# Optimization experiments

Hardware: AMD Instinct MI355X
Metric: run time of the kernel (lower is better)

## Reference

```python
import jax, jax.numpy as jnp
import numpy as np

# RoIAlign config (matches init_kwargs)
OUT_H = OUT_W = 7
SPATIAL_SCALE = 0.25
SAMPLING_RATIO = 2  # fixed grid per bin (aligned=True, detectron2-style)
N_IMG, C, H, W = 2, 256, 200, 304
N_ROIS = 512


def setup_inputs() -> dict:
    key = jax.random.key(0)
    kf, kb, kx1, ky1, kw, kh = jax.random.split(key, 6)
    features = jax.random.normal(kf, (N_IMG, C, H, W), dtype=jnp.float32)
    # rois: [R,5] = (batch_idx, x1, y1, x2, y2) in input-image coords (image ~ 1216x800)
    bidx = jax.random.randint(kb, (N_ROIS,), 0, N_IMG).astype(jnp.float32)
    x1 = jax.random.uniform(kx1, (N_ROIS,), minval=0.0, maxval=1100.0)
    y1 = jax.random.uniform(ky1, (N_ROIS,), minval=0.0, maxval=700.0)
    bw = jax.random.uniform(kw, (N_ROIS,), minval=8.0, maxval=116.0)
    bh = jax.random.uniform(kh, (N_ROIS,), minval=8.0, maxval=100.0)
    rois = jnp.stack([bidx, x1, y1, x1 + bw, y1 + bh], axis=1).astype(jnp.float32)
    return {"features": features, "rois": rois}


def roi_align(features, rois):
    N, C_, H_, W_ = features.shape
    G = SAMPLING_RATIO
    b = rois[:, 0].astype(jnp.int32)
    # aligned=True: scale then shift by -0.5 (continuous pixel model)
    x1 = rois[:, 1] * SPATIAL_SCALE - 0.5
    y1 = rois[:, 2] * SPATIAL_SCALE - 0.5
    x2 = rois[:, 3] * SPATIAL_SCALE - 0.5
    y2 = rois[:, 4] * SPATIAL_SCALE - 0.5
    roi_w = x2 - x1  # aligned: no clamp to min 1
    roi_h = y2 - y1
    bin_w = roi_w / OUT_W
    bin_h = roi_h / OUT_H

    # sample coordinates: per roi, OUT*G points along each axis
    iy = jnp.arange(OUT_H * G)
    ix = jnp.arange(OUT_W * G)
    # y = y1 + ph*bin_h + (s+0.5)*bin_h/G
    ys = y1[:, None] + (iy // G) * bin_h[:, None] + ((iy % G) + 0.5) * bin_h[:, None] / G  # [R, OUT_H*G]
    xs = x1[:, None] + (ix // G) * bin_w[:, None] + ((ix % G) + 0.5) * bin_w[:, None] / G  # [R, OUT_W*G]

    y = ys[:, :, None]  # [R, Py, 1]
    x = xs[:, None, :]  # [R, 1, Px]
    valid = ((y > -1.0) & (y < H_) & (x > -1.0) & (x < W_)).astype(features.dtype)  # [R,Py,Px]

    yc = jnp.clip(y, 0.0, H_ - 1)
    xc = jnp.clip(x, 0.0, W_ - 1)
    y0 = jnp.floor(yc).astype(jnp.int32)
    x0 = jnp.floor(xc).astype(jnp.int32)
    y1i = jnp.minimum(y0 + 1, H_ - 1)
    x1i = jnp.minimum(x0 + 1, W_ - 1)
    ly = yc - y0
    lx = xc - x0
    hy = 1.0 - ly
    hx = 1.0 - lx

    badv = b[:, None, None]
    Py, Px = OUT_H * G, OUT_W * G
    y0b = jnp.broadcast_to(y0, (rois.shape[0], Py, Px))
    y1b = jnp.broadcast_to(y1i, (rois.shape[0], Py, Px))
    x0b = jnp.broadcast_to(x0, (rois.shape[0], Py, Px))
    x1b = jnp.broadcast_to(x1i, (rois.shape[0], Py, Px))

    # advanced indexing: [R,Py,Px,C]
    v00 = features[badv, :, y0b, x0b]
    v01 = features[badv, :, y0b, x1b]
    v10 = features[badv, :, y1b, x0b]
    v11 = features[badv, :, y1b, x1b]

    w00 = (hy * hx) * valid
    w01 = (hy * lx) * valid
    w10 = (ly * hx) * valid
    w11 = (ly * lx) * valid

    samp = (w00[..., None] * v00 + w01[..., None] * v01 +
            w10[..., None] * v10 + w11[..., None] * v11)  # [R,Py,Px,C]
    # average pool over the GxG samples per bin
    R = rois.shape[0]
    out = samp.reshape(R, OUT_H, G, OUT_W, G, C_).mean(axis=(2, 4))  # [R,OUT_H,OUT_W,C]
    return jnp.transpose(out, (0, 3, 1, 2))  # [R,C,OUT_H,OUT_W]


def reference(features, rois):
    return roi_align(features, rois)
```

## Files before the change

### kernel.cpp

```cpp
#include <hip/hip_runtime.h>


#define OUT_H 7
#define OUT_W 7
constexpr float SPATIAL_SCALE = 0.25f;
constexpr int CN = 256;
constexpr int FH = 200;
constexpr int FW = 304;
constexpr int N_IMG = 2;
constexpr int N_ROIS = 512;
constexpr int PIX = FH * FW;
constexpr size_t PLANE = (size_t)PIX;
constexpr size_t NHWC_ELEMS = (size_t)N_IMG * PLANE * CN;
constexpr size_t NHWC_BF16_BYTES = NHWC_ELEMS * sizeof(unsigned short);

constexpr int CT = 64;
constexpr int PT = 128;

__device__ __forceinline__ unsigned short f2bf_rne(float f) {
    unsigned int u = __float_as_uint(f);
    unsigned int r = (u + 0x7FFFu + ((u >> 16) & 1u)) >> 16;
    return (unsigned short)r;
}

__global__ __launch_bounds__(256) void nchw_to_nhwc_bf16_tiled(
    const float* __restrict__ in, unsigned short* __restrict__ ws)
{
    const int pbase = blockIdx.x * PT;
    const int nc = blockIdx.y;
    const int n = nc >> 2;
    const int cbase = (nc & 3) * CT;

    __shared__ float tile[CT][PT + 1];

    {
        const int q = threadIdx.x & 31;
        const int r = threadIdx.x >> 5;
        const float* src = in + ((size_t)n * CN + cbase) * PLANE + pbase + 4 * q;
#pragma unroll
        for (int i = 0; i < 8; ++i) {
            const int c = r + 8 * i;
            const float4 v = *(const float4*)(src + (size_t)c * PLANE);
            tile[c][4 * q + 0] = v.x;
            tile[c][4 * q + 1] = v.y;
            tile[c][4 * q + 2] = v.z;
            tile[c][4 * q + 3] = v.w;
        }
    }
    __syncthreads();
    {
        const int cq = threadIdx.x & 7;
        const int p0 = threadIdx.x >> 3;
        unsigned short* dstbase =
            ws + ((size_t)n * PLANE + pbase) * CN + cbase + 8 * cq;
#pragma unroll
        for (int i2 = 0; i2 < 4; ++i2) {
            const int p = p0 + 32 * i2;
            uint4 pk;
            pk.x = (unsigned int)f2bf_rne(tile[8 * cq + 0][p]) |
                   ((unsigned int)f2bf_rne(tile[8 * cq + 1][p]) << 16);
            pk.y = (unsigned int)f2bf_rne(tile[8 * cq + 2][p]) |
                   ((unsigned int)f2bf_rne(tile[8 * cq + 3][p]) << 16);
            pk.z = (unsigned int)f2bf_rne(tile[8 * cq + 4][p]) |
                   ((unsigned int)f2bf_rne(tile[8 * cq + 5][p]) << 16);
            pk.w = (unsigned int)f2bf_rne(tile[8 * cq + 6][p]) |
                   ((unsigned int)f2bf_rne(tile[8 * cq + 7][p]) << 16);
            *(uint4*)(dstbase + (size_t)p * CN) = pk;
        }
    }
}

__global__ __launch_bounds__(128) void roi_align_nhwc_bf16(
    const unsigned short* __restrict__ ws,
    const float* __restrict__ rois,
    float* __restrict__ out)
{
    const int b = blockIdx.x;
    const int x = b & 7;
    const int sid = b >> 3;
    const int half = sid & 1;
    const int ph = (sid >> 1) % 7;
    const int r  = ((sid >> 1) / 7) * 8 + x;
    const int t  = threadIdx.x;

    __shared__ float s_roi[5];
    __shared__ int   s_off[16][4];
    __shared__ float s_w[16][4];
    __shared__ int   s_b;

    if (t < 5) s_roi[t] = rois[r * 5 + t];
    __syncthreads();

    const int NW = half ? 6 : 8;
    const int NS = 2 * NW;
    if (t < NS) {
        const int gy  = (t >= NW) ? 1 : 0;
        const int ixl = t - gy * NW;
        const int ix  = half * 8 + ixl;
        const float x1 = s_roi[1] * SPATIAL_SCALE - 0.5f;
        const float y1 = s_roi[2] * SPATIAL_SCALE - 0.5f;
        const float x2 = s_roi[3] * SPATIAL_SCALE - 0.5f;
        const float y2 = s_roi[4] * SPATIAL_SCALE - 0.5f;
        const float bin_w = (x2 - x1) / OUT_W;
        const float bin_h = (y2 - y1) / OUT_H;
        const float y = y1 + ph * bin_h + (gy + 0.5f) * bin_h * 0.5f;
        const float xf = x1 + (ix >> 1) * bin_w + ((ix & 1) + 0.5f) * bin_w * 0.5f;
        const float validf =
            (y > -1.0f && y < (float)FH && xf > -1.0f && xf < (float)FW) ? 1.0f : 0.0f;
        const float yc = fminf(fmaxf(y, 0.0f), (float)(FH - 1));
        const float xc = fminf(fmaxf(xf, 0.0f), (float)(FW - 1));
        const int y0 = (int)floorf(yc);
        const int x0 = (int)floorf(xc);
        const int y1i = min(y0 + 1, FH - 1);
        const int x1i = min(x0 + 1, FW - 1);
        const float ly = yc - (float)y0;
        const float lx = xc - (float)x0;
        const float hy = 1.0f - ly;
        const float hx = 1.0f - lx;
        s_off[t][0] = ((y0  * FW + x0 ) * CN) * 2;
        s_off[t][1] = ((y0  * FW + x1i) * CN) * 2;
        s_off[t][2] = ((y1i * FW + x0 ) * CN) * 2;
        s_off[t][3] = ((y1i * FW + x1i) * CN) * 2;
        s_w[t][0] = hy * hx * validf;
        s_w[t][1] = hy * lx * validf;
        s_w[t][2] = ly * hx * validf;
        s_w[t][3] = ly * lx * validf;
    }
    if (t == 0) s_b = (int)s_roi[0];
    __syncthreads();

    const char* base =
        (const char*)(ws + (size_t)s_b * (PLANE * CN) + 2 * t);

    float acc0[4] = {0.f, 0.f, 0.f, 0.f};
    float acc1[4] = {0.f, 0.f, 0.f, 0.f};

    if (half == 0) {
#pragma unroll
        for (int s = 0; s < 16; ++s) {
            const int pw = (s & 7) >> 1;
#pragma unroll
            for (int k = 0; k < 4; ++k) {
                const unsigned int u = *(const unsigned int*)(base + s_off[s][k]);
                const float f0 = __uint_as_float(u << 16);
                const float f1 = __uint_as_float(u & 0xFFFF0000u);
                const float w = s_w[s][k];
                acc0[pw] = fmaf(w, f0, acc0[pw]);
                acc1[pw] = fmaf(w, f1, acc1[pw]);
            }
        }
    } else {
#pragma unroll
        for (int s = 0; s < 12; ++s) {
            const int pw = (s % 6) >> 1;
#pragma unroll
            for (int k = 0; k < 4; ++k) {
                const unsigned int u = *(const unsigned int*)(base + s_off[s][k]);
                const float f0 = __uint_as_float(u << 16);
                const float f1 = __uint_as_float(u & 0xFFFF0000u);
                const float w = s_w[s][k];
                acc0[pw] = fmaf(w, f0, acc0[pw]);
                acc1[pw] = fmaf(w, f1, acc1[pw]);
            }
        }
    }

    const int pw0 = half ? 4 : 0;
    const int npw = half ? 3 : 4;
    const size_t outbase = ((size_t)r * CN + 2 * t) * (OUT_H * OUT_W)
                         + (size_t)ph * OUT_W + pw0;
    for (int pw = 0; pw < npw; ++pw) {
        out[outbase + pw] = acc0[pw] * 0.25f;
        out[outbase + (OUT_H * OUT_W) + pw] = acc1[pw] * 0.25f;
    }
}

__global__ __launch_bounds__(256) void roi_align_nchw(
    const float* __restrict__ feat,
    const float* __restrict__ rois,
    float* __restrict__ out)
{
    const int r  = blockIdx.x;
    const int ph = blockIdx.y;
    const int c  = threadIdx.x;

    __shared__ float s_roi[5];
    __shared__ int   s_off[28][4];
    __shared__ float s_w[28][4];
    __shared__ int   s_b;

    if (threadIdx.x < 5) s_roi[threadIdx.x] = rois[r * 5 + threadIdx.x];
    __syncthreads();

    if (threadIdx.x < 28) {
        const int s  = threadIdx.x;
        const int gy = s / 14;
        const int ix = s % 14;
        const float x1 = s_roi[1] * SPATIAL_SCALE - 0.5f;
        const float y1 = s_roi[2] * SPATIAL_SCALE - 0.5f;
        const float x2 = s_roi[3] * SPATIAL_SCALE - 0.5f;
        const float y2 = s_roi[4] * SPATIAL_SCALE - 0.5f;
        const float bin_w = (x2 - x1) / OUT_W;
        const float bin_h = (y2 - y1) / OUT_H;
        const float y = y1 + ph * bin_h + (gy + 0.5f) * bin_h * 0.5f;
        const float xf = x1 + (ix >> 1) * bin_w + ((ix & 1) + 0.5f) * bin_w * 0.5f;
        const float validf =
            (y > -1.0f && y < (float)FH && xf > -1.0f && xf < (float)FW) ? 1.0f : 0.0f;
        const float yc = fminf(fmaxf(y, 0.0f), (float)(FH - 1));
        const float xc = fminf(fmaxf(xf, 0.0f), (float)(FW - 1));
        const int y0 = (int)floorf(yc);
        const int x0 = (int)floorf(xc);
        const int y1i = min(y0 + 1, FH - 1);
        const int x1i = min(x0 + 1, FW - 1);
        const float ly = yc - (float)y0;
        const float lx = xc - (float)x0;
        const float hy = 1.0f - ly;
        const float hx = 1.0f - lx;
        s_off[s][0] = y0  * FW + x0;
        s_off[s][1] = y0  * FW + x1i;
        s_off[s][2] = y1i * FW + x0;
        s_off[s][3] = y1i * FW + x1i;
        s_w[s][0] = hy * hx * validf;
        s_w[s][1] = hy * lx * validf;
        s_w[s][2] = ly * hx * validf;
        s_w[s][3] = ly * lx * validf;
    }
    if (threadIdx.x == 0) s_b = (int)s_roi[0];
    __syncthreads();

    const float* base = feat + ((size_t)s_b * CN + c) * PLANE;

    float acc[OUT_W] = {0.f, 0.f, 0.f, 0.f, 0.f, 0.f, 0.f};
#pragma unroll
    for (int s = 0; s < 28; ++s) {
        const float v0 = base[s_off[s][0]];
        const float v1 = base[s_off[s][1]];
        const float v2 = base[s_off[s][2]];
        const float v3 = base[s_off[s][3]];
        acc[(s % 14) >> 1] += s_w[s][0] * v0 + s_w[s][1] * v1 +
                              s_w[s][2] * v2 + s_w[s][3] * v3;
    }

    const size_t outbase = ((size_t)r * CN + c) * (OUT_H * OUT_W) + (size_t)ph * OUT_W;
#pragma unroll
    for (int pw = 0; pw < OUT_W; ++pw) {
        out[outbase + pw] = acc[pw] * 0.25f;
    }
}

extern "C" void kernel_launch(void* const* d_in, const int* in_sizes, int n_in,
                              void* d_out, int out_size, void* d_ws, size_t ws_size,
                              hipStream_t stream) {
    const float* feat = (const float*)d_in[0];
    const float* rois = (const float*)d_in[1];
    float* out = (float*)d_out;

    if (ws_size >= NHWC_BF16_BYTES) {
        unsigned short* ws = (unsigned short*)d_ws;
        dim3 tgrid(PIX / PT, (N_IMG * CN) / CT, 1);
        nchw_to_nhwc_bf16_tiled<<<tgrid, dim3(256, 1, 1), 0, stream>>>(feat, ws);
        roi_align_nhwc_bf16<<<dim3(N_ROIS * OUT_H * 2, 1, 1), dim3(128, 1, 1), 0, stream>>>(
            ws, rois, out);
    } else {
        dim3 grid(N_ROIS, OUT_H, 1);
        roi_align_nchw<<<grid, dim3(256, 1, 1), 0, stream>>>(feat, rois, out);
    }
}
```

Measured before the change: 234.6 us.

## Process two output rows and four channels per thread in RoIAlign kernel

```diff
diff --git a/kernel.cpp b/kernel.cpp
--- a/kernel.cpp
+++ b/kernel.cpp
@@ -70,7 +70,7 @@
     }
 }
 
-__global__ __launch_bounds__(128) void roi_align_nhwc_bf16(
+__global__ __launch_bounds__(64) void roi_align_nhwc_bf16(
     const unsigned short* __restrict__ ws,
     const float* __restrict__ rois,
     float* __restrict__ out)
@@ -78,25 +78,26 @@
     const int b = blockIdx.x;
     const int x = b & 7;
     const int sid = b >> 3;
-    const int half = sid & 1;
-    const int ph = (sid >> 1) % 7;
-    const int r  = ((sid >> 1) / 7) * 8 + x;
+    const int r    = (sid >> 2) * 8 + x;
+    const int pair = sid & 3;
+    const int ph0  = 2 * pair;
     const int t  = threadIdx.x;
 
     __shared__ float s_roi[5];
-    __shared__ int   s_off[16][4];
-    __shared__ float s_w[16][4];
+    __shared__ int   s_off[56][4];
+    __shared__ float s_w[56][4];
     __shared__ int   s_b;
 
     if (t < 5) s_roi[t] = rois[r * 5 + t];
     __syncthreads();
 
-    const int NW = half ? 6 : 8;
-    const int NS = 2 * NW;
+    const int NS = (pair < 3) ? 56 : 28;
     if (t < NS) {
-        const int gy  = (t >= NW) ? 1 : 0;
-        const int ixl = t - gy * NW;
-        const int ix  = half * 8 + ixl;
+        const int row = t / 28;
+        const int ss  = t % 28;
+        const int gy = ss / 14;
+        const int ix = ss % 14;
+        const int ph = ph0 + row;
         const float x1 = s_roi[1] * SPATIAL_SCALE - 0.5f;
         const float y1 = s_roi[2] * SPATIAL_SCALE - 0.5f;
         const float x2 = s_roi[3] * SPATIAL_SCALE - 0.5f;
@@ -130,48 +131,69 @@
     __syncthreads();
 
     const char* base =
-        (const char*)(ws + (size_t)s_b * (PLANE * CN) + 2 * t);
-
-    float acc0[4] = {0.f, 0.f, 0.f, 0.f};
-    float acc1[4] = {0.f, 0.f, 0.f, 0.f};
-
-    if (half == 0) {
-#pragma unroll
-        for (int s = 0; s < 16; ++s) {
-            const int pw = (s & 7) >> 1;
+        (const char*)(ws + (size_t)s_b * (PLANE * CN)) + 8 * t;
+
+    float acc0[14] = {0.f,0.f,0.f,0.f,0.f,0.f,0.f,0.f,0.f,0.f,0.f,0.f,0.f,0.f};
+    float acc1[14] = {0.f,0.f,0.f,0.f,0.f,0.f,0.f,0.f,0.f,0.f,0.f,0.f,0.f,0.f};
+    float acc2[14] = {0.f,0.f,0.f,0.f,0.f,0.f,0.f,0.f,0.f,0.f,0.f,0.f,0.f,0.f};
+    float acc3[14] = {0.f,0.f,0.f,0.f,0.f,0.f,0.f,0.f,0.f,0.f,0.f,0.f,0.f,0.f};
+
+    if (pair < 3) {
+#pragma unroll
+        for (int s = 0; s < 56; ++s) {
+            const int ai = (s / 28) * 7 + (((s % 28) % 14) >> 1);
 #pragma unroll
             for (int k = 0; k < 4; ++k) {
-                const unsigned int u = *(const unsigned int*)(base + s_off[s][k]);
-                const float f0 = __uint_as_float(u << 16);
-                const float f1 = __uint_as_float(u & 0xFFFF0000u);
+                const uint2 u = *(const uint2*)(base + s_off[s][k]);
+                const float f0 = __uint_as_float(u.x << 16);
+                const float f1 = __uint_as_float(u.x & 0xFFFF0000u);
+                const float f2 = __uint_as_float(u.y << 16);
+                const float f3 = __uint_as_float(u.y & 0xFFFF0000u);
                 const float w = s_w[s][k];
-                acc0[pw] = fmaf(w, f0, acc0[pw]);
-                acc1[pw] = fmaf(w, f1, acc1[pw]);
+                acc0[ai] = fmaf(w, f0, acc0[ai]);
+                acc1[ai] = fmaf(w, f1, acc1[ai]);
+                acc2[ai] = fmaf(w, f2, acc2[ai]);
+                acc3[ai] = fmaf(w, f3, acc3[ai]);
             }
         }
     } else {
 #pragma unroll
-        for (int s = 0; s < 12; ++s) {
-            const int pw = (s % 6) >> 1;
+        for (int s = 0; s < 28; ++s) {
+            const int ai = (s % 14) >> 1;
 #pragma unroll
             for (int k = 0; k < 4; ++k) {
-                const unsigned int u = *(const unsigned int*)(base + s_off[s][k]);
-                const float f0 = __uint_as_float(u << 16);
-                const float f1 = __uint_as_float(u & 0xFFFF0000u);
+                const uint2 u = *(const uint2*)(base + s_off[s][k]);
+                const float f0 = __uint_as_float(u.x << 16);
+                const float f1 = __uint_as_float(u.x & 0xFFFF0000u);
+                const float f2 = __uint_as_float(u.y << 16);
+                const float f3 = __uint_as_float(u.y & 0xFFFF0000u);
                 const float w = s_w[s][k];
-                acc0[pw] = fmaf(w, f0, acc0[pw]);
-                acc1[pw] = fmaf(w, f1, acc1[pw]);
+                acc0[ai] = fmaf(w, f0, acc0[ai]);
+                acc1[ai] = fmaf(w, f1, acc1[ai]);
+                acc2[ai] = fmaf(w, f2, acc2[ai]);
+                acc3[ai] = fmaf(w, f3, acc3[ai]);
             }
         }
     }
 
-    const int pw0 = half ? 4 : 0;
-    const int npw = half ? 3 : 4;
-    const size_t outbase = ((size_t)r * CN + 2 * t) * (OUT_H * OUT_W)
-                         + (size_t)ph * OUT_W + pw0;
-    for (int pw = 0; pw < npw; ++pw) {
-        out[outbase + pw] = acc0[pw] * 0.25f;
-        out[outbase + (OUT_H * OUT_W) + pw] = acc1[pw] * 0.25f;
+    constexpr int OHW = OUT_H * OUT_W;
+    const size_t outbase = ((size_t)r * CN + 4 * t) * OHW + (size_t)ph0 * OUT_W;
+    if (pair < 3) {
+#pragma unroll
+        for (int i = 0; i < 14; ++i) {
+            out[outbase + 0 * OHW + i] = acc0[i] * 0.25f;
+            out[outbase + 1 * OHW + i] = acc1[i] * 0.25f;
+            out[outbase + 2 * OHW + i] = acc2[i] * 0.25f;
+            out[outbase + 3 * OHW + i] = acc3[i] * 0.25f;
+        }
+    } else {
+#pragma unroll
+        for (int i = 0; i < 7; ++i) {
+            out[outbase + 0 * OHW + i] = acc0[i] * 0.25f;
+            out[outbase + 1 * OHW + i] = acc1[i] * 0.25f;
+            out[outbase + 2 * OHW + i] = acc2[i] * 0.25f;
+            out[outbase + 3 * OHW + i] = acc3[i] * 0.25f;
+        }
     }
 }
 
@@ -259,7 +281,7 @@
         unsigned short* ws = (unsigned short*)d_ws;
         dim3 tgrid(PIX / PT, (N_IMG * CN) / CT, 1);
         nchw_to_nhwc_bf16_tiled<<<tgrid, dim3(256, 1, 1), 0, stream>>>(feat, ws);
-        roi_align_nhwc_bf16<<<dim3(N_ROIS * OUT_H * 2, 1, 1), dim3(128, 1, 1), 0, stream>>>(
+        roi_align_nhwc_bf16<<<dim3(N_ROIS * 4, 1, 1), dim3(64, 1, 1), 0, stream>>>(
             ws, rois, out);
     } else {
         dim3 grid(N_ROIS, OUT_H, 1);
```

Measured after the change: 232.5 us. Within noise of the previous version (-0.9%).
